# Kernel optimization log

Measured on AMD Instinct MI355X. Metric: run time of the kernel, lower is better.

Reference implementation:

```python
import jax, jax.numpy as jnp
import numpy as np
from jax import lax


def setup_inputs() -> dict:
    key = jax.random.key(0)
    k1, k2, k3 = jax.random.split(key, 3)
    B, T, D, K = 64, 512, 1024, 32
    x = jax.random.normal(k1, (B, T, D), dtype=jnp.float32)
    W = jax.random.normal(k2, (D, K), dtype=jnp.float32) * (1.0 / np.sqrt(D))
    U = jax.random.normal(k3, (K, K), dtype=jnp.float32) * 0.1
    b = jnp.zeros((K,), dtype=jnp.float32)
    return {"x": x, "W": W, "U": U, "b": b}


def _crf_marginals(x, W, U, b):
    # Emission (input) energies: linear activation of x @ W + b -> [B, T, K]
    e = jnp.einsum('btd,dk->btk', x, W) + b
    e_t = jnp.swapaxes(e, 0, 1)  # [T, B, K]

    # Forward recursion: alpha_t = logsumexp_prev(alpha_{t-1} + U) + e_t
    def fwd_step(alpha, et):
        a = jax.nn.logsumexp(alpha[:, :, None] + U[None, :, :], axis=1) + et
        return a, a

    alpha0 = e_t[0]
    _, alphas = lax.scan(fwd_step, alpha0, e_t[1:])
    alpha = jnp.concatenate([alpha0[None], alphas], axis=0)  # [T, B, K]

    # Backward recursion: beta_t = logsumexp_next(U + e_{t+1} + beta_{t+1})
    def bwd_step(beta, et_next):
        nb = jax.nn.logsumexp(U[None, :, :] + (et_next + beta)[:, None, :], axis=2)
        return nb, nb

    betaT = jnp.zeros_like(alpha0)
    _, betas = lax.scan(bwd_step, betaT, e_t[1:], reverse=True)
    beta = jnp.concatenate([betas, betaT[None]], axis=0)  # [T, B, K]

    # Marginal probability of each tag at each timestep
    marg = jax.nn.softmax(alpha + beta, axis=-1)  # [T, B, K]
    return jnp.swapaxes(marg, 0, 1)  # [B, T, K]


def reference(x, W, U, b):
    return _crf_marginals(x, W, U, b)
```

## Files before the change

### kernel.cpp

```cpp
#include <hip/hip_runtime.h>
#include <stdint.h>

#define TT 512
#define BB 64
#define DD 1024
#define KK 32

typedef __attribute__((ext_vector_type(8))) short short8v;
typedef __attribute__((ext_vector_type(4))) float f4v;

__device__ __forceinline__ float rfl(float v) {
  return __int_as_float(__builtin_amdgcn_readfirstlane(__float_as_int(v)));
}

__device__ __forceinline__ void gload_lds16(const float4* g, float4* l) {
  __builtin_amdgcn_global_load_lds(
      (const __attribute__((address_space(1))) uint32_t*)g,
      (__attribute__((address_space(3))) uint32_t*)l, 16, 0, 0);
}

__device__ __forceinline__ void cvt2(float f0, float f1,
                                     unsigned& h, unsigned& lo) {
  unsigned u0 = __float_as_uint(f0), u1 = __float_as_uint(f1);
  h = (u1 & 0xFFFF0000u) | (u0 >> 16);
  float r0 = f0 - __uint_as_float(u0 & 0xFFFF0000u);
  float r1 = f1 - __uint_as_float(u1 & 0xFFFF0000u);
  lo = (__float_as_uint(r1) & 0xFFFF0000u) | (__float_as_uint(r0) >> 16);
}

__global__ __launch_bounds__(256) void wconv_kernel(
    const float* __restrict__ W, uint4* __restrict__ Wf) {
  const int t = blockIdx.x * 256 + threadIdx.x;
  const int l = t & 63;
  const int kt = (t >> 6) & 1;
  const int c = t >> 7;
  const int d0 = c * 32 + (l >> 4) * 8;
  const int k = kt * 16 + (l & 15);
  unsigned h[4], q[4];
#pragma unroll
  for (int j = 0; j < 4; ++j) {
    float f0 = W[(size_t)(d0 + 2 * j) * KK + k];
    float f1 = W[(size_t)(d0 + 2 * j + 1) * KK + k];
    cvt2(f0, f1, h[j], q[j]);
  }
  Wf[(size_t)(c * 4 + kt * 2 + 0) * 64 + l] = make_uint4(h[0], h[1], h[2], h[3]);
  Wf[(size_t)(c * 4 + kt * 2 + 1) * 64 + l] = make_uint4(q[0], q[1], q[2], q[3]);
}

__global__ __launch_bounds__(256) void emit_kernel(
    const float* __restrict__ x, const uint4* __restrict__ Wf,
    const float* __restrict__ bias, float* __restrict__ F) {
  __shared__ float4 Ls4[1024];
  const int t = threadIdx.x;
  const int l = t & 63;
  const int w = t >> 6;
  const int m0 = blockIdx.x * 64;
  const int base_r = m0 + w * 16;

  float4* Lxw = &Ls4[w * 256];

  const float *xs0, *xs1;
  {
    int s = l;       int row = s >> 3; int v = (s & 7) ^ (row & 7);
    xs0 = x + (size_t)(base_r + row) * DD + v * 4;
  }
  {
    int s = 64 + l;  int row = s >> 3; int v = (s & 7) ^ (row & 7);
    xs1 = x + (size_t)(base_r + row) * DD + v * 4;
  }

  const int r_ = l & 15, dg_ = l >> 4;
  const int slot0 = r_ * 8 + ((dg_ * 2) ^ (r_ & 7));
  const int slot1 = r_ * 8 + ((dg_ * 2 + 1) ^ (r_ & 7));

  const uint4* Wp = Wf + l;

  f4v acc0 = {0.f, 0.f, 0.f, 0.f};
  f4v acc1 = {0.f, 0.f, 0.f, 0.f};

#define STAGE(c, p) do {                                                     \
    gload_lds16((const float4*)(xs0 + (c) * 32), Lxw + (p) * 128);           \
    gload_lds16((const float4*)(xs1 + (c) * 32), Lxw + (p) * 128 + 64);      \
  } while (0)

#define LOADW(c, w0, w1, w2, w3) do {                                        \
    w0 = Wp[(size_t)((c) * 4 + 0) * 64];                                     \
    w1 = Wp[(size_t)((c) * 4 + 1) * 64];                                     \
    w2 = Wp[(size_t)((c) * 4 + 2) * 64];                                     \
    w3 = Wp[(size_t)((c) * 4 + 3) * 64];                                     \
  } while (0)

#define COMPUTE(p, wh0, wl0, wh1, wl1) do {                                  \
    float4 a0 = Lxw[(p) * 128 + slot0];                                      \
    float4 a1 = Lxw[(p) * 128 + slot1];                                      \
    unsigned h0, h1, h2, h3, q0, q1, q2, q3;                                 \
    cvt2(a0.x, a0.y, h0, q0); cvt2(a0.z, a0.w, h1, q1);                      \
    cvt2(a1.x, a1.y, h2, q2); cvt2(a1.z, a1.w, h3, q3);                      \
    uint4 ahu = make_uint4(h0, h1, h2, h3);                                  \
    uint4 alu = make_uint4(q0, q1, q2, q3);                                  \
    short8v Ah = __builtin_bit_cast(short8v, ahu);                           \
    short8v Al = __builtin_bit_cast(short8v, alu);                           \
    short8v Bh0 = __builtin_bit_cast(short8v, wh0);                          \
    short8v Bl0 = __builtin_bit_cast(short8v, wl0);                          \
    short8v Bh1 = __builtin_bit_cast(short8v, wh1);                          \
    short8v Bl1 = __builtin_bit_cast(short8v, wl1);                          \
    acc0 = __builtin_amdgcn_mfma_f32_16x16x32_bf16(Ah, Bh0, acc0, 0, 0, 0);  \
    acc1 = __builtin_amdgcn_mfma_f32_16x16x32_bf16(Ah, Bh1, acc1, 0, 0, 0);  \
    acc0 = __builtin_amdgcn_mfma_f32_16x16x32_bf16(Al, Bh0, acc0, 0, 0, 0);  \
    acc1 = __builtin_amdgcn_mfma_f32_16x16x32_bf16(Al, Bh1, acc1, 0, 0, 0);  \
    acc0 = __builtin_amdgcn_mfma_f32_16x16x32_bf16(Ah, Bl0, acc0, 0, 0, 0);  \
    acc1 = __builtin_amdgcn_mfma_f32_16x16x32_bf16(Ah, Bl1, acc1, 0, 0, 0);  \
  } while (0)

  uint4 wa0, wa1, wa2, wa3;
  uint4 wb0, wb1, wb2, wb3;

  STAGE(0, 0);
  LOADW(0, wa0, wa1, wa2, wa3);
  STAGE(1, 1);
  LOADW(1, wb0, wb1, wb2, wb3);

#pragma unroll 1
  for (int c = 0; c < 30; c += 2) {
    asm volatile("s_waitcnt vmcnt(6)" ::: "memory");
    COMPUTE(0, wa0, wa1, wa2, wa3);
    asm volatile("" ::: "memory");
    STAGE(c + 2, 0);
    LOADW(c + 2, wa0, wa1, wa2, wa3);
    asm volatile("s_waitcnt vmcnt(6)" ::: "memory");
    COMPUTE(1, wb0, wb1, wb2, wb3);
    asm volatile("" ::: "memory");
    STAGE(c + 3, 1);
    LOADW(c + 3, wb0, wb1, wb2, wb3);
  }
  asm volatile("s_waitcnt vmcnt(6)" ::: "memory");
  COMPUTE(0, wa0, wa1, wa2, wa3);
  asm volatile("s_waitcnt vmcnt(0)" ::: "memory");
  COMPUTE(1, wb0, wb1, wb2, wb3);

#undef STAGE
#undef LOADW
#undef COMPUTE

  const int col = l & 15;
  const int rb = base_r + (l >> 4) * 4;
  const float b0 = bias[col];
  const float b1 = bias[col + 16];
#pragma unroll
  for (int j = 0; j < 4; ++j) {
    F[(size_t)(rb + j) * KK + col]      = __expf(acc0[j] + b0);
    F[(size_t)(rb + j) * KK + col + 16] = __expf(acc1[j] + b1);
  }
}

__global__ __launch_bounds__(64) void scan_kernel(
    const float* __restrict__ F, const float* __restrict__ U,
    float* __restrict__ A, float* __restrict__ Bw) {
  __shared__ __align__(16) float cur[KK];
  const int l = threadIdx.x;
  const int kk = l & 31;
  const int h = l >> 5;
  const int seg = blockIdx.x & 15;
  const int b = (blockIdx.x >> 4) & 63;
  const int dir = blockIdx.x >> 10;

  const float* Fb = F + (size_t)b * TT * KK;
  float V[16];

  if (dir == 0) {
    float* Ab = A + (size_t)b * TT * KK;
#pragma unroll
    for (int j = 0; j < 16; ++j) V[j] = __expf(U[(h * 16 + j) * KK + kk]);
    const int lo = seg * 32, hi = seg * 32 + 31;
    const int t0 = (seg == 0) ? 0 : lo - 17;
    float a = Fb[t0 * KK + kk];
    cur[kk] = a;
    if (seg == 0 && l < 32) Ab[l] = a;
    __builtin_amdgcn_wave_barrier();

#define FSTEP(fv, tcur)                                                     \
    {                                                                       \
      const float4* c4 = (const float4*)cur;                                \
      float4 y0 = c4[h*4+0], y1 = c4[h*4+1], y2 = c4[h*4+2], y3 = c4[h*4+3];\
      float r = __builtin_amdgcn_rcpf(rfl(y0.x));                           \
      float s0 = fmaf(y0.x, V[0],  fmaf(y0.y, V[1],                         \
                 fmaf(y0.z, V[2],  y0.w * V[3])));                          \
      float s1 = fmaf(y1.x, V[4],  fmaf(y1.y, V[5],                         \
                 fmaf(y1.z, V[6],  y1.w * V[7])));                          \
      float s2 = fmaf(y2.x, V[8],  fmaf(y2.y, V[9],                         \
                 fmaf(y2.z, V[10], y2.w * V[11])));                         \
      float s3 = fmaf(y3.x, V[12], fmaf(y3.y, V[13],                        \
                 fmaf(y3.z, V[14], y3.w * V[15])));                         \
      float s = (s0 + s1) + (s2 + s3);                                      \
      s += __shfl_xor(s, 32);                                               \
      a = s * ((fv) * r);                                                   \
      cur[kk] = a;                                                          \
      __builtin_amdgcn_wave_barrier();                                      \
      if ((tcur) >= lo && l < 32) Ab[(tcur) * KK + l] = a;                  \
    }

    int t = t0 + 1;
    float f0 = Fb[t * KK + kk],       f1 = Fb[(t + 1) * KK + kk];
    float f2 = Fb[(t + 2) * KK + kk], f3 = Fb[(t + 3) * KK + kk];
    for (; t + 3 <= hi; t += 4) {
      int tn = t + 4;
      int u0 = tn     > hi ? hi : tn;
      int u1 = tn + 1 > hi ? hi : tn + 1;
      int u2 = tn + 2 > hi ? hi : tn + 2;
      int u3 = tn + 3 > hi ? hi : tn + 3;
      float n0 = Fb[u0 * KK + kk], n1 = Fb[u1 * KK + kk];
      float n2 = Fb[u2 * KK + kk], n3 = Fb[u3 * KK + kk];
      FSTEP(f0, t); FSTEP(f1, t + 1); FSTEP(f2, t + 2); FSTEP(f3, t + 3);
      f0 = n0; f1 = n1; f2 = n2; f3 = n3;
    }
    if (t <= hi) { FSTEP(f0, t); ++t; }
    if (t <= hi) { FSTEP(f1, t); ++t; }
    if (t <= hi) { FSTEP(f2, t); ++t; }
#undef FSTEP
  } else {
    const int b2 = b;
    float* Bb = Bw + (size_t)b2 * TT * KK;
#pragma unroll
    for (int j = 0; j < 16; ++j) V[j] = __expf(U[kk * KK + h * 16 + j]);
    const int lo = seg * 32;
    const int hs = seg * 32 + 31;
    const int t1 = (seg == 15) ? (TT - 1) : (lo + 48);
    float g = Fb[t1 * KK + kk];
    cur[kk] = g;
    if (seg == 15 && l < 32) Bb[(TT - 1) * KK + l] = 1.0f;
    __builtin_amdgcn_wave_barrier();

#define BSTEP(fv, tcur)                                                     \
    {                                                                       \
      const float4* c4 = (const float4*)cur;                                \
      float4 y0 = c4[h*4+0], y1 = c4[h*4+1], y2 = c4[h*4+2], y3 = c4[h*4+3];\
      float r = __builtin_amdgcn_rcpf(rfl(y0.x));                           \
      float s0 = fmaf(y0.x, V[0],  fmaf(y0.y, V[1],                         \
                 fmaf(y0.z, V[2],  y0.w * V[3])));                          \
      float s1 = fmaf(y1.x, V[4],  fmaf(y1.y, V[5],                         \
                 fmaf(y1.z, V[6],  y1.w * V[7])));                          \
      float s2 = fmaf(y2.x, V[8],  fmaf(y2.y, V[9],                         \
                 fmaf(y2.z, V[10], y2.w * V[11])));                         \
      float s3 = fmaf(y3.x, V[12], fmaf(y3.y, V[13],                        \
                 fmaf(y3.z, V[14], y3.w * V[15])));                         \
      float s = (s0 + s1) + (s2 + s3);                                      \
      s += __shfl_xor(s, 32);                                               \
      float bnew = s * r;                                                   \
      g = bnew * (fv);                                                      \
      cur[kk] = g;                                                          \
      __builtin_amdgcn_wave_barrier();                                      \
      if ((tcur) <= hs && l < 32) Bb[(tcur) * KK + l] = bnew;               \
    }

    int t = t1 - 1;
    float f0 = Fb[t * KK + kk],       f1 = Fb[(t - 1) * KK + kk];
    float f2 = Fb[(t - 2) * KK + kk], f3 = Fb[(t - 3) * KK + kk];
    for (; t - 3 >= lo; t -= 4) {
      int tn = t - 4;
      int u0 = tn     < 0 ? 0 : tn;
      int u1 = tn - 1 < 0 ? 0 : tn - 1;
      int u2 = tn - 2 < 0 ? 0 : tn - 2;
      int u3 = tn - 3 < 0 ? 0 : tn - 3;
      float n0 = Fb[u0 * KK + kk], n1 = Fb[u1 * KK + kk];
      float n2 = Fb[u2 * KK + kk], n3 = Fb[u3 * KK + kk];
      BSTEP(f0, t); BSTEP(f1, t - 1); BSTEP(f2, t - 2); BSTEP(f3, t - 3);
      f0 = n0; f1 = n1; f2 = n2; f3 = n3;
    }
    if (t >= lo) { BSTEP(f0, t); --t; }
    if (t >= lo) { BSTEP(f1, t); --t; }
    if (t >= lo) { BSTEP(f2, t); --t; }
#undef BSTEP
  }
}

__global__ __launch_bounds__(256) void combine_kernel(
    const float* __restrict__ Bw, float* __restrict__ out) {
  size_t i = (size_t)blockIdx.x * 256 + threadIdx.x;
  float p = out[i] * Bw[i];
  float ssum = p;
  ssum += __shfl_xor(ssum, 1);
  ssum += __shfl_xor(ssum, 2);
  ssum += __shfl_xor(ssum, 4);
  ssum += __shfl_xor(ssum, 8);
  ssum += __shfl_xor(ssum, 16);
  out[i] = p / ssum;
}

extern "C" void kernel_launch(void* const* d_in, const int* in_sizes, int n_in,
                              void* d_out, int out_size, void* d_ws, size_t ws_size,
                              hipStream_t stream) {
  const float* x = (const float*)d_in[0];
  const float* W = (const float*)d_in[1];
  const float* U = (const float*)d_in[2];
  const float* b = (const float*)d_in[3];
  float* out = (float*)d_out;
  float* F = (float*)d_ws;
  float* Bw = F + (size_t)BB * TT * KK;
  uint4* Wf = (uint4*)(Bw + (size_t)BB * TT * KK);

  wconv_kernel<<<16, 256, 0, stream>>>(W, Wf);
  emit_kernel<<<512, 256, 0, stream>>>(x, Wf, b, F);
  scan_kernel<<<2048, 64, 0, stream>>>(F, U, out, Bw);
  combine_kernel<<<(BB * TT * KK) / 256, 256, 0, stream>>>(Bw, out);
}
```

Measured before the change: 224.9 us.

## Split emission GEMM K-dimension across warps with direct register loads

```diff
diff --git a/kernel.cpp b/kernel.cpp
--- a/kernel.cpp
+++ b/kernel.cpp
@@ -11,12 +11,6 @@
 
 __device__ __forceinline__ float rfl(float v) {
   return __int_as_float(__builtin_amdgcn_readfirstlane(__float_as_int(v)));
-}
-
-__device__ __forceinline__ void gload_lds16(const float4* g, float4* l) {
-  __builtin_amdgcn_global_load_lds(
-      (const __attribute__((address_space(1))) uint32_t*)g,
-      (__attribute__((address_space(3))) uint32_t*)l, 16, 0, 0);
 }
 
 __device__ __forceinline__ void cvt2(float f0, float f1,
@@ -47,109 +41,86 @@
   Wf[(size_t)(c * 4 + kt * 2 + 1) * 64 + l] = make_uint4(q[0], q[1], q[2], q[3]);
 }
 
-__global__ __launch_bounds__(256) void emit_kernel(
+__global__ __launch_bounds__(256, 4) void emit_kernel(
     const float* __restrict__ x, const uint4* __restrict__ Wf,
     const float* __restrict__ bias, float* __restrict__ F) {
-  __shared__ float4 Ls4[1024];
+  __shared__ float Ls[4 * 64 * 8];
   const int t = threadIdx.x;
   const int l = t & 63;
   const int w = t >> 6;
-  const int m0 = blockIdx.x * 64;
-  const int base_r = m0 + w * 16;
-
-  float4* Lxw = &Ls4[w * 256];
-
-  const float *xs0, *xs1;
-  {
-    int s = l;       int row = s >> 3; int v = (s & 7) ^ (row & 7);
-    xs0 = x + (size_t)(base_r + row) * DD + v * 4;
-  }
-  {
-    int s = 64 + l;  int row = s >> 3; int v = (s & 7) ^ (row & 7);
-    xs1 = x + (size_t)(base_r + row) * DD + v * 4;
-  }
-
-  const int r_ = l & 15, dg_ = l >> 4;
-  const int slot0 = r_ * 8 + ((dg_ * 2) ^ (r_ & 7));
-  const int slot1 = r_ * 8 + ((dg_ * 2 + 1) ^ (r_ & 7));
-
+  const int rt = w >> 1;
+  const int h = w & 1;
+  const int m0 = blockIdx.x * 32;
+  const int base_r = m0 + rt * 16;
+
+  const float* xp = x + (size_t)(base_r + (l & 15)) * DD + h * 512 + (l >> 4) * 8;
   const uint4* Wp = Wf + l;
 
   f4v acc0 = {0.f, 0.f, 0.f, 0.f};
   f4v acc1 = {0.f, 0.f, 0.f, 0.f};
 
-#define STAGE(c, p) do {                                                     \
-    gload_lds16((const float4*)(xs0 + (c) * 32), Lxw + (p) * 128);           \
-    gload_lds16((const float4*)(xs1 + (c) * 32), Lxw + (p) * 128 + 64);      \
-  } while (0)
-
-#define LOADW(c, w0, w1, w2, w3) do {                                        \
-    w0 = Wp[(size_t)((c) * 4 + 0) * 64];                                     \
-    w1 = Wp[(size_t)((c) * 4 + 1) * 64];                                     \
-    w2 = Wp[(size_t)((c) * 4 + 2) * 64];                                     \
-    w3 = Wp[(size_t)((c) * 4 + 3) * 64];                                     \
-  } while (0)
-
-#define COMPUTE(p, wh0, wl0, wh1, wl1) do {                                  \
-    float4 a0 = Lxw[(p) * 128 + slot0];                                      \
-    float4 a1 = Lxw[(p) * 128 + slot1];                                      \
-    unsigned h0, h1, h2, h3, q0, q1, q2, q3;                                 \
-    cvt2(a0.x, a0.y, h0, q0); cvt2(a0.z, a0.w, h1, q1);                      \
-    cvt2(a1.x, a1.y, h2, q2); cvt2(a1.z, a1.w, h3, q3);                      \
-    uint4 ahu = make_uint4(h0, h1, h2, h3);                                  \
-    uint4 alu = make_uint4(q0, q1, q2, q3);                                  \
-    short8v Ah = __builtin_bit_cast(short8v, ahu);                           \
-    short8v Al = __builtin_bit_cast(short8v, alu);                           \
-    short8v Bh0 = __builtin_bit_cast(short8v, wh0);                          \
-    short8v Bl0 = __builtin_bit_cast(short8v, wl0);                          \
-    short8v Bh1 = __builtin_bit_cast(short8v, wh1);                          \
-    short8v Bl1 = __builtin_bit_cast(short8v, wl1);                          \
-    acc0 = __builtin_amdgcn_mfma_f32_16x16x32_bf16(Ah, Bh0, acc0, 0, 0, 0);  \
-    acc1 = __builtin_amdgcn_mfma_f32_16x16x32_bf16(Ah, Bh1, acc1, 0, 0, 0);  \
-    acc0 = __builtin_amdgcn_mfma_f32_16x16x32_bf16(Al, Bh0, acc0, 0, 0, 0);  \
-    acc1 = __builtin_amdgcn_mfma_f32_16x16x32_bf16(Al, Bh1, acc1, 0, 0, 0);  \
-    acc0 = __builtin_amdgcn_mfma_f32_16x16x32_bf16(Ah, Bl0, acc0, 0, 0, 0);  \
-    acc1 = __builtin_amdgcn_mfma_f32_16x16x32_bf16(Ah, Bl1, acc1, 0, 0, 0);  \
-  } while (0)
-
-  uint4 wa0, wa1, wa2, wa3;
-  uint4 wb0, wb1, wb2, wb3;
-
-  STAGE(0, 0);
-  LOADW(0, wa0, wa1, wa2, wa3);
-  STAGE(1, 1);
-  LOADW(1, wb0, wb1, wb2, wb3);
-
-#pragma unroll 1
-  for (int c = 0; c < 30; c += 2) {
-    asm volatile("s_waitcnt vmcnt(6)" ::: "memory");
-    COMPUTE(0, wa0, wa1, wa2, wa3);
-    asm volatile("" ::: "memory");
-    STAGE(c + 2, 0);
-    LOADW(c + 2, wa0, wa1, wa2, wa3);
-    asm volatile("s_waitcnt vmcnt(6)" ::: "memory");
-    COMPUTE(1, wb0, wb1, wb2, wb3);
-    asm volatile("" ::: "memory");
-    STAGE(c + 3, 1);
-    LOADW(c + 3, wb0, wb1, wb2, wb3);
-  }
-  asm volatile("s_waitcnt vmcnt(6)" ::: "memory");
-  COMPUTE(0, wa0, wa1, wa2, wa3);
-  asm volatile("s_waitcnt vmcnt(0)" ::: "memory");
-  COMPUTE(1, wb0, wb1, wb2, wb3);
-
-#undef STAGE
-#undef LOADW
-#undef COMPUTE
-
-  const int col = l & 15;
-  const int rb = base_r + (l >> 4) * 4;
-  const float b0 = bias[col];
-  const float b1 = bias[col + 16];
-#pragma unroll
-  for (int j = 0; j < 4; ++j) {
-    F[(size_t)(rb + j) * KK + col]      = __expf(acc0[j] + b0);
-    F[(size_t)(rb + j) * KK + col + 16] = __expf(acc1[j] + b1);
+  float4 xa[4][2];
+  uint4 wv[2][4];
+#pragma unroll
+  for (int i = 0; i < 4; ++i) {
+    xa[i][0] = *(const float4*)(xp + i * 32);
+    xa[i][1] = *(const float4*)(xp + i * 32 + 4);
+  }
+#pragma unroll
+  for (int i = 0; i < 2; ++i)
+#pragma unroll
+    for (int j = 0; j < 4; ++j)
+      wv[i][j] = Wp[(size_t)((h * 16 + i) * 4 + j) * 64];
+
+#pragma unroll
+  for (int c = 0; c < 16; ++c) {
+    const float4 a0 = xa[c & 3][0];
+    const float4 a1 = xa[c & 3][1];
+    unsigned h0, h1, h2, h3, q0, q1, q2, q3;
+    cvt2(a0.x, a0.y, h0, q0); cvt2(a0.z, a0.w, h1, q1);
+    cvt2(a1.x, a1.y, h2, q2); cvt2(a1.z, a1.w, h3, q3);
+    const uint4 ahu = make_uint4(h0, h1, h2, h3);
+    const uint4 alu = make_uint4(q0, q1, q2, q3);
+    const short8v Ah = __builtin_bit_cast(short8v, ahu);
+    const short8v Al = __builtin_bit_cast(short8v, alu);
+    const short8v Bh0 = __builtin_bit_cast(short8v, wv[c & 1][0]);
+    const short8v Bl0 = __builtin_bit_cast(short8v, wv[c & 1][1]);
+    const short8v Bh1 = __builtin_bit_cast(short8v, wv[c & 1][2]);
+    const short8v Bl1 = __builtin_bit_cast(short8v, wv[c & 1][3]);
+    if (c + 4 < 16) {
+      xa[c & 3][0] = *(const float4*)(xp + (c + 4) * 32);
+      xa[c & 3][1] = *(const float4*)(xp + (c + 4) * 32 + 4);
+    }
+    if (c + 2 < 16) {
+#pragma unroll
+      for (int j = 0; j < 4; ++j)
+        wv[c & 1][j] = Wp[(size_t)((h * 16 + c + 2) * 4 + j) * 64];
+    }
+    acc0 = __builtin_amdgcn_mfma_f32_16x16x32_bf16(Ah, Bh0, acc0, 0, 0, 0);
+    acc1 = __builtin_amdgcn_mfma_f32_16x16x32_bf16(Ah, Bh1, acc1, 0, 0, 0);
+    acc0 = __builtin_amdgcn_mfma_f32_16x16x32_bf16(Al, Bh0, acc0, 0, 0, 0);
+    acc1 = __builtin_amdgcn_mfma_f32_16x16x32_bf16(Al, Bh1, acc1, 0, 0, 0);
+    acc0 = __builtin_amdgcn_mfma_f32_16x16x32_bf16(Ah, Bl0, acc0, 0, 0, 0);
+    acc1 = __builtin_amdgcn_mfma_f32_16x16x32_bf16(Ah, Bl1, acc1, 0, 0, 0);
+  }
+
+  {
+    float* qp = Ls + (w * 64 + l) * 8;
+#pragma unroll
+    for (int j = 0; j < 4; ++j) { qp[j] = acc0[j]; qp[4 + j] = acc1[j]; }
+  }
+  __syncthreads();
+  if (h == 0) {
+    const float* p2 = Ls + ((w + 1) * 64 + l) * 8;
+    const int col = l & 15;
+    const int rb = base_r + (l >> 4) * 4;
+    const float b0 = bias[col];
+    const float b1 = bias[col + 16];
+#pragma unroll
+    for (int j = 0; j < 4; ++j) {
+      F[(size_t)(rb + j) * KK + col]      = __expf(acc0[j] + p2[j]     + b0);
+      F[(size_t)(rb + j) * KK + col + 16] = __expf(acc1[j] + p2[4 + j] + b1);
+    }
   }
 }
 
@@ -299,7 +270,7 @@
   uint4* Wf = (uint4*)(Bw + (size_t)BB * TT * KK);
 
   wconv_kernel<<<16, 256, 0, stream>>>(W, Wf);
-  emit_kernel<<<512, 256, 0, stream>>>(x, Wf, b, F);
+  emit_kernel<<<1024, 256, 0, stream>>>(x, Wf, b, F);
   scan_kernel<<<2048, 64, 0, stream>>>(F, U, out, Bw);
   combine_kernel<<<(BB * TT * KK) / 256, 256, 0, stream>>>(Bw, out);
 }
```

Result: faster. 218.5 us (-2.8%).
